# Optimization experiments

Measured on AMD Instinct MI355X. Metric: run time of the kernel, lower is better.

Reference implementation:

```python
import jax, jax.numpy as jnp
import numpy as np

B, T, H = 8, 4096, 512
K = 8192  # codebook size


def setup_inputs() -> dict:
    key = jax.random.key(0)
    kz, ke = jax.random.split(key)
    z = jax.random.normal(kz, (B, T, H), dtype=jnp.float32)
    emb = jax.random.normal(ke, (K, H), dtype=jnp.float32) * 0.02
    return {"z": z, "emb": emb}


def reference(z, emb):
    b, t, h = z.shape
    flat = z.reshape(b * t, h)
    dist = (jnp.sum(flat * flat, axis=1, keepdims=True)
            - 2.0 * (flat @ emb.T)
            + jnp.sum(emb * emb, axis=1)[None, :])
    idx = jnp.argmin(dist, axis=1)            # (b*t,)
    z_q = emb[idx].reshape(b, t, h)           # codebook lookup
    # straight-through estimator
    z_st = z + jax.lax.stop_gradient(z_q - z)
    codebook_loss = jnp.mean((z_q - jax.lax.stop_gradient(z)) ** 2)
    commit_loss = jnp.mean((z - jax.lax.stop_gradient(z_q)) ** 2)
    return z_st, idx.reshape(b, t), codebook_loss, commit_loss
```

## Files before the change

kernel.cpp:

```cpp
#include <hip/hip_runtime.h>
#include <cstdint>
#include <cstddef>

#define M_ROWS 32768
#define K_CODES 8192
#define H_DIM 512
#define TAU 2.5e-4f
#define MAXFLAG 32768

typedef float  f32x4 __attribute__((ext_vector_type(4)));
typedef short  s16x8 __attribute__((ext_vector_type(8)));

typedef __attribute__((address_space(3))) void as3_void;
typedef const __attribute__((address_space(1))) void as1_cvoid;
#define GLD16(gp, lp) __builtin_amdgcn_global_load_lds((as1_cvoid*)(gp), (as3_void*)(lp), 16, 0, 0)

__device__ __forceinline__ unsigned short f2bf(float f) {
    uint32_t u = __float_as_uint(f);
    u = u + 0x7fffu + ((u >> 16) & 1u);
    return (unsigned short)(u >> 16);
}
__device__ __forceinline__ float bf2f(unsigned short h) {
    return __uint_as_float(((uint32_t)h) << 16);
}

__device__ __forceinline__ float np_sumsq_row32(const float* row, int lane32) {
    const int c = lane32 >> 3, j = lane32 & 7;
    const float* p = row + c * 128 + j;
    float s = __fmul_rn(p[0], p[0]);
    #pragma unroll
    for (int t = 1; t < 16; ++t) {
        const float v = p[8 * t];
        s = __fadd_rn(s, __fmul_rn(v, v));
    }
    s = __fadd_rn(s, __shfl_xor(s, 1));
    s = __fadd_rn(s, __shfl_xor(s, 2));
    s = __fadd_rn(s, __shfl_xor(s, 4));
    s = __fadd_rn(s, __shfl_xor(s, 8));
    s = __fadd_rn(s, __shfl_xor(s, 16));
    return s;
}

__global__ __launch_bounds__(256) void prep_kernel(
    const float* __restrict__ z, const float* __restrict__ emb,
    unsigned short* __restrict__ zh, unsigned short* __restrict__ zl,
    unsigned short* __restrict__ eh, unsigned short* __restrict__ el,
    float* __restrict__ x2, float* __restrict__ e2,
    float* __restrict__ loss_slots, int* __restrict__ flag_count, int do_split)
{
    __shared__ float zr[8][512];
    const int row0 = blockIdx.x * 8;

    #pragma unroll
    for (int k = 0; k < 4; ++k) {
        const int f  = threadIdx.x + k * 256;
        const int r  = f >> 7;
        const int c4 = f & 127;
        const int grow = row0 + r;
        const float* src; unsigned short* hi; unsigned short* lo; size_t off;
        if (grow < M_ROWS) { src = z;   hi = zh; lo = zl; off = (size_t)grow * H_DIM; }
        else               { src = emb; hi = eh; lo = el; off = (size_t)(grow - M_ROWS) * H_DIM; }
        const float4 v = *reinterpret_cast<const float4*>(src + off + (size_t)c4 * 4);
        zr[r][c4 * 4 + 0] = v.x;
        zr[r][c4 * 4 + 1] = v.y;
        zr[r][c4 * 4 + 2] = v.z;
        zr[r][c4 * 4 + 3] = v.w;
        if (do_split) {
            ushort4 h, l;
            h.x = f2bf(v.x); l.x = f2bf(v.x - bf2f(h.x));
            h.y = f2bf(v.y); l.y = f2bf(v.y - bf2f(h.y));
            h.z = f2bf(v.z); l.z = f2bf(v.z - bf2f(h.z));
            h.w = f2bf(v.w); l.w = f2bf(v.w - bf2f(h.w));
            *reinterpret_cast<ushort4*>(hi + off + (size_t)c4 * 4) = h;
            *reinterpret_cast<ushort4*>(lo + off + (size_t)c4 * 4) = l;
        }
    }
    __syncthreads();

    const int r = threadIdx.x >> 5;
    const float s = np_sumsq_row32(&zr[r][0], threadIdx.x & 31);
    if ((threadIdx.x & 31) == 0) {
        const int grow = row0 + r;
        if (grow < M_ROWS) x2[grow] = s;
        else               e2[grow - M_ROWS] = s;
    }
    if (blockIdx.x == 0) {
        if (threadIdx.x < 2) loss_slots[threadIdx.x] = 0.f;
        if (threadIdx.x == 0) *flag_count = 0;
    }
}

__device__ __forceinline__ void top2_merge(float& b1, int& ix, float& b2,
                                           float ob1, int oix, float ob2) {
    if (ob1 < b1)      { b2 = fminf(b1, ob2); b1 = ob1; ix = oix; }
    else if (ob1 > b1) { b2 = fminf(b2, ob1); }
    else               { if (oix < ix) ix = oix; b2 = b1; }
}

__global__ __launch_bounds__(512, 1) void mfma_dist_kernel(
    const unsigned short* __restrict__ zh, const unsigned short* __restrict__ zl,
    const unsigned short* __restrict__ eh, const unsigned short* __restrict__ el,
    const float* __restrict__ x2, const float* __restrict__ e2,
    float* __restrict__ pb1, float* __restrict__ pb2, int* __restrict__ pidx)
{
    __shared__ __align__(16) unsigned short lb[2][4][8192];

    const int tid = threadIdx.x;
    const int l   = tid & 63;
    const int w   = tid >> 6;
    const int wm  = w >> 2;
    const int wn  = w & 3;

    const int bid  = blockIdx.x;
    const int xcd  = bid & 7;
    const int sq   = bid >> 3;
    const int band = sq >> 7;
    const int r128 = sq & 127;
    const int ct   = r128 >> 2;
    const int rt   = (band * 8 + xcd) * 4 + (r128 & 3);
    const int row0 = rt * 256;
    const int c0   = ct * 256;

    const int m    = w >> 1;
    const int half = w & 1;
    const unsigned short* sp = (m == 0) ? zh : (m == 1) ? zl : (m == 2) ? eh : el;
    const int rbase0 = (m < 2) ? row0 : c0;
    const unsigned short* sb = sp
        + (size_t)(rbase0 + half * 128 + (l >> 2)) * H_DIM
        + ((l & 3) ^ ((l >> 3) & 3)) * 8;

    const int aoff = (wm * 128 + (l & 15)) * 64 + (((l >> 4) ^ ((l >> 1) & 3)) * 16);
    const int boff = (wn * 64  + (l & 15)) * 64 + (((l >> 4) ^ ((l >> 1) & 3)) * 16);

    f32x4 acc[8][4];
    #pragma unroll
    for (int i = 0; i < 8; ++i)
        #pragma unroll
        for (int j = 0; j < 4; ++j)
            acc[i][j] = (f32x4){0.f, 0.f, 0.f, 0.f};

    {
        char* dst = (char*)&lb[0][m][0] + half * 8192;
        #pragma unroll
        for (int t = 0; t < 8; ++t)
            GLD16(sb + (size_t)t * 16 * H_DIM, dst + t * 1024);
    }
    asm volatile("s_waitcnt vmcnt(0)" ::: "memory");
    __builtin_amdgcn_s_barrier();

    for (int s = 0; s < 16; ++s) {
        const int par = s & 1;

        if (s < 15) {
            const unsigned short* src = sb + (s + 1) * 32;
            char* dst = (char*)&lb[par ^ 1][m][0] + half * 8192;
            #pragma unroll
            for (int t = 0; t < 8; ++t)
                GLD16(src + (size_t)t * 16 * H_DIM, dst + t * 1024);
            asm volatile("s_waitcnt vmcnt(8)" ::: "memory");
        } else {
            asm volatile("s_waitcnt vmcnt(0)" ::: "memory");
        }
        __builtin_amdgcn_s_barrier();

        const char* pAh = (const char*)&lb[par][0][0];
        const char* pAl = (const char*)&lb[par][1][0];
        const char* pBh = (const char*)&lb[par][2][0];
        const char* pBl = (const char*)&lb[par][3][0];

        s16x8 ah[8];
        #pragma unroll
        for (int i = 0; i < 8; ++i)
            ah[i] = *(const s16x8*)(pAh + aoff + i * 1024);
        s16x8 bh[4], bv[4];
        #pragma unroll
        for (int j = 0; j < 4; ++j) {
            bh[j] = *(const s16x8*)(pBh + boff + j * 1024);
            bv[j] = *(const s16x8*)(pBl + boff + j * 1024);
        }

        __builtin_amdgcn_s_setprio(1);
        #pragma unroll
        for (int j = 0; j < 4; ++j)
            #pragma unroll
            for (int i = 0; i < 8; ++i)
                acc[i][j] = __builtin_amdgcn_mfma_f32_16x16x32_bf16(ah[i], bv[j], acc[i][j], 0, 0, 0);
        s16x8 avA[4];
        #pragma unroll
        for (int i = 0; i < 4; ++i)
            avA[i] = *(const s16x8*)(pAl + aoff + i * 1024);
        #pragma unroll
        for (int j = 0; j < 4; ++j)
            #pragma unroll
            for (int i = 0; i < 8; ++i)
                acc[i][j] = __builtin_amdgcn_mfma_f32_16x16x32_bf16(ah[i], bh[j], acc[i][j], 0, 0, 0);
        s16x8 avB[4];
        #pragma unroll
        for (int i = 0; i < 4; ++i)
            avB[i] = *(const s16x8*)(pAl + aoff + (4 + i) * 1024);
        #pragma unroll
        for (int j = 0; j < 4; ++j)
            #pragma unroll
            for (int i = 0; i < 4; ++i)
                acc[i][j] = __builtin_amdgcn_mfma_f32_16x16x32_bf16(avA[i], bh[j], acc[i][j], 0, 0, 0);
        #pragma unroll
        for (int j = 0; j < 4; ++j)
            #pragma unroll
            for (int i = 0; i < 4; ++i)
                acc[4 + i][j] = __builtin_amdgcn_mfma_f32_16x16x32_bf16(avB[i], bh[j], acc[4 + i][j], 0, 0, 0);
        __builtin_amdgcn_s_setprio(0);

        __builtin_amdgcn_s_barrier();
    }

    float* mb1 = (float*)&lb[0][0][0];
    float* mb2 = mb1 + 1024;
    int*   mi  = (int*)(mb1 + 2048);

    float e2v[4];
    #pragma unroll
    for (int j = 0; j < 4; ++j)
        e2v[j] = e2[c0 + wn * 64 + j * 16 + (l & 15)];

    #pragma unroll
    for (int i = 0; i < 8; ++i) {
        const float4 x2v = *reinterpret_cast<const float4*>(
            x2 + row0 + wm * 128 + i * 16 + (l >> 4) * 4);
        const float x2a[4] = {x2v.x, x2v.y, x2v.z, x2v.w};
        #pragma unroll
        for (int r = 0; r < 4; ++r) {
            float b1 = 3.4e38f, b2 = 3.4e38f; int ix = 0;
            #pragma unroll
            for (int j = 0; j < 4; ++j) {
                const float d = __fadd_rn(__fmaf_rn(-2.f, acc[i][j][r], x2a[r]), e2v[j]);
                const int cj = c0 + wn * 64 + j * 16 + (l & 15);
                if (d < b1)      { b2 = b1; b1 = d; ix = cj; }
                else if (d < b2) { b2 = d; }
            }
            #pragma unroll
            for (int mm = 1; mm <= 8; mm <<= 1) {
                const float ob1 = __shfl_xor(b1, mm);
                const float ob2 = __shfl_xor(b2, mm);
                const int   oix = __shfl_xor(ix, mm);
                top2_merge(b1, ix, b2, ob1, oix, ob2);
            }
            if ((l & 15) == 0) {
                const int rl = wm * 128 + i * 16 + (l >> 4) * 4 + r;
                mb1[wn * 256 + rl] = b1;
                mb2[wn * 256 + rl] = b2;
                mi [wn * 256 + rl] = ix;
            }
        }
    }
    __syncthreads();
    if (tid < 256) {
        float b1 = mb1[tid], b2 = mb2[tid]; int ix = mi[tid];
        #pragma unroll
        for (int q = 1; q < 4; ++q)
            top2_merge(b1, ix, b2, mb1[q * 256 + tid], mi[q * 256 + tid], mb2[q * 256 + tid]);
        const size_t o = (size_t)ct * M_ROWS + row0 + tid;
        pb1[o] = b1; pb2[o] = b2; pidx[o] = ix;
    }
}

__global__ __launch_bounds__(256) void combine_kernel(
    const float* __restrict__ pb1, const float* __restrict__ pb2,
    const int* __restrict__ pidx,
    int* __restrict__ idx_i, float* __restrict__ idx_f,
    int* __restrict__ flag_count, int* __restrict__ flag_rows)
{
    const int r = blockIdx.x * 256 + threadIdx.x;
    if (r >= M_ROWS) return;
    float b1 = pb1[r], b2 = pb2[r]; int ix = pidx[r];
    #pragma unroll 4
    for (int ct = 1; ct < 32; ++ct)
        top2_merge(b1, ix, b2, pb1[(size_t)ct * M_ROWS + r],
                   pidx[(size_t)ct * M_ROWS + r], pb2[(size_t)ct * M_ROWS + r]);
    idx_i[r] = ix;
    idx_f[r] = (float)ix;
    if (b2 - b1 < TAU) {
        const int p = atomicAdd(flag_count, 1);
        if (p < MAXFLAG) flag_rows[p] = r;
    }
}

#define BM 64
#define BN 128
#define BH 32
#define PADZ 4
#define PADE 4

__device__ __forceinline__ void stage_transposed(const float* __restrict__ src,
                                                 int row0, int h0,
                                                 float* lds, int R, int ldp) {
    const int nf4 = R * (BH / 4);
    for (int f = threadIdx.x; f < nf4; f += 256) {
        const int r  = f / (BH / 4);
        const int c4 = (f % (BH / 4)) * 4;
        const float4 v = *reinterpret_cast<const float4*>(
            src + (size_t)(row0 + r) * H_DIM + h0 + c4);
        lds[(c4 + 0) * ldp + r] = v.x;
        lds[(c4 + 1) * ldp + r] = v.y;
        lds[(c4 + 2) * ldp + r] = v.z;
        lds[(c4 + 3) * ldp + r] = v.w;
    }
}

__global__ __launch_bounds__(256) void dist_argmin_kernel(
    const float* __restrict__ z, const float* __restrict__ emb,
    const float* __restrict__ x2, const float* __restrict__ e2,
    int* __restrict__ idx_i, float* __restrict__ idx_f,
    int* __restrict__ flag_count, int* __restrict__ flag_rows)
{
    __shared__ float zs[BH * (BM + PADZ)];
    __shared__ float es[BH * (BN + PADE)];
    __shared__ float bd[BM][17];
    __shared__ float bd2[BM][17];
    __shared__ int   bi[BM][17];

    const int row0 = blockIdx.x * BM;
    const int tx = threadIdx.x & 15;
    const int ty = threadIdx.x >> 4;

    float x2r[4];
    #pragma unroll
    for (int i = 0; i < 4; ++i) x2r[i] = x2[row0 + ty * 4 + i];

    float best[4], best2[4];
    int   bidx[4];
    #pragma unroll
    for (int i = 0; i < 4; ++i) { best[i] = 3.4e38f; best2[i] = 3.4e38f; bidx[i] = 0; }

    for (int nt = 0; nt < K_CODES / BN; ++nt) {
        float acc[4][8];
        #pragma unroll
        for (int i = 0; i < 4; ++i)
            #pragma unroll
            for (int j = 0; j < 8; ++j) acc[i][j] = 0.f;

        for (int hc = 0; hc < H_DIM / BH; ++hc) {
            __syncthreads();
            stage_transposed(z,   row0,    hc * BH, zs, BM, BM + PADZ);
            stage_transposed(emb, nt * BN, hc * BH, es, BN, BN + PADE);
            __syncthreads();
            #pragma unroll
            for (int h = 0; h < BH; ++h) {
                const float4 zr = *reinterpret_cast<const float4*>(&zs[h * (BM + PADZ) + ty * 4]);
                const float4 e0 = *reinterpret_cast<const float4*>(&es[h * (BN + PADE) + tx * 4]);
                const float4 e1 = *reinterpret_cast<const float4*>(&es[h * (BN + PADE) + 64 + tx * 4]);
                const float zrv[4] = {zr.x, zr.y, zr.z, zr.w};
                const float ev[8]  = {e0.x, e0.y, e0.z, e0.w, e1.x, e1.y, e1.z, e1.w};
                #pragma unroll
                for (int i = 0; i < 4; ++i)
                    #pragma unroll
                    for (int j = 0; j < 8; ++j)
                        acc[i][j] = fmaf(zrv[i], ev[j], acc[i][j]);
            }
        }
        #pragma unroll
        for (int j = 0; j < 8; ++j) {
            const int code = nt * BN + (j < 4 ? tx * 4 + j : 64 + tx * 4 + (j - 4));
            const float e2v = e2[code];
            #pragma unroll
            for (int i = 0; i < 4; ++i) {
                const float d = __fadd_rn(__fmaf_rn(-2.f, acc[i][j], x2r[i]), e2v);
                if (d < best[i])       { best2[i] = best[i]; best[i] = d; bidx[i] = code; }
                else if (d < best2[i]) { best2[i] = d; }
            }
        }
    }

    __syncthreads();
    #pragma unroll
    for (int i = 0; i < 4; ++i) {
        bd [ty * 4 + i][tx] = best[i];
        bd2[ty * 4 + i][tx] = best2[i];
        bi [ty * 4 + i][tx] = bidx[i];
    }
    __syncthreads();
    if (threadIdx.x < BM) {
        const int r = threadIdx.x;
        float g1 = bd[r][0]; int gi = bi[r][0]; float g2 = bd2[r][0];
        #pragma unroll
        for (int t = 1; t < 16; ++t) {
            const float v = bd[r][t]; const int x = bi[r][t];
            if (v < g1)       { g2 = g1; g1 = v; gi = x; }
            else if (v == g1) { g2 = g1; if (x < gi) gi = x; }
            else              { g2 = fminf(g2, v); }
            g2 = fminf(g2, bd2[r][t]);
        }
        idx_i[row0 + r] = gi;
        idx_f[row0 + r] = (float)gi;
        if (g2 - g1 < TAU) {
            const int p = atomicAdd(flag_count, 1);
            if (p < MAXFLAG) flag_rows[p] = row0 + r;
        }
    }
}

__global__ __launch_bounds__(256) void fixup_scan_kernel(
    const float* __restrict__ z, const float* __restrict__ emb,
    const float* __restrict__ x2, const float* __restrict__ e2,
    const int* __restrict__ flag_count, const int* __restrict__ flag_rows,
    float* __restrict__ qb1, int* __restrict__ qix)
{
    __shared__ float zrow[H_DIM];
    __shared__ float sd[256];
    __shared__ int   si[256];
    int n = *flag_count; if (n > MAXFLAG) n = MAXFLAG;
    const int q = blockIdx.x & 3;
    for (int j = blockIdx.x >> 2; j < n; j += (gridDim.x >> 2)) {
        const int row = flag_rows[j];
        __syncthreads();
        for (int h = threadIdx.x; h < H_DIM; h += 256)
            zrow[h] = z[(size_t)row * H_DIM + h];
        __syncthreads();
        const float x2r = x2[row];
        float bdv = 3.4e38f; int biv = 0x7fffffff;
        for (int k = q * 2048 + threadIdx.x; k < q * 2048 + 2048; k += 256) {
            const float* ek = emb + (size_t)k * H_DIM;
            double d0 = 0.0, d1 = 0.0, d2 = 0.0, d3 = 0.0;
            for (int h = 0; h < H_DIM; h += 4) {
                const float4 ev = *reinterpret_cast<const float4*>(ek + h);
                const float4 zv = *reinterpret_cast<const float4*>(&zrow[h]);
                d0 = fma((double)zv.x, (double)ev.x, d0);
                d1 = fma((double)zv.y, (double)ev.y, d1);
                d2 = fma((double)zv.z, (double)ev.z, d2);
                d3 = fma((double)zv.w, (double)ev.w, d3);
            }
            const float gf = (float)((d0 + d1) + (d2 + d3));
            const float d = __fadd_rn(__fmaf_rn(-2.f, gf, x2r), e2[k]);
            if (d < bdv) { bdv = d; biv = k; }
        }
        sd[threadIdx.x] = bdv; si[threadIdx.x] = biv;
        __syncthreads();
        for (int s = 128; s; s >>= 1) {
            if (threadIdx.x < s) {
                const float od = sd[threadIdx.x + s]; const int oi = si[threadIdx.x + s];
                if (od < sd[threadIdx.x] ||
                    (od == sd[threadIdx.x] && oi < si[threadIdx.x])) {
                    sd[threadIdx.x] = od; si[threadIdx.x] = oi;
                }
            }
            __syncthreads();
        }
        if (threadIdx.x == 0) { qb1[j * 4 + q] = sd[0]; qix[j * 4 + q] = si[0]; }
        __syncthreads();
    }
}

__global__ __launch_bounds__(256) void fixup_merge_kernel(
    const int* __restrict__ flag_count, const int* __restrict__ flag_rows,
    const float* __restrict__ qb1, const int* __restrict__ qix,
    int* __restrict__ idx_i, float* __restrict__ idx_f)
{
    int n = *flag_count; if (n > MAXFLAG) n = MAXFLAG;
    const int t = blockIdx.x * 256 + threadIdx.x;
    if (t >= n) return;
    float b = qb1[t * 4]; int ix = qix[t * 4];
    #pragma unroll
    for (int q = 1; q < 4; ++q) {
        const float ob = qb1[t * 4 + q];
        if (ob < b) { b = ob; ix = qix[t * 4 + q]; }
    }
    idx_i[flag_rows[t]] = ix;
    idx_f[flag_rows[t]] = (float)ix;
}

__global__ __launch_bounds__(256) void epilogue_kernel(
    const float* __restrict__ z, const float* __restrict__ emb,
    const int* __restrict__ idx_i,
    float* __restrict__ z_st, float* __restrict__ loss_slots)
{
    const int NQ = M_ROWS * (H_DIM / 4);
    const float4* z4 = reinterpret_cast<const float4*>(z);
    const float4* e4 = reinterpret_cast<const float4*>(emb);
    float4* o4 = reinterpret_cast<float4*>(z_st);
    float local = 0.f;
    for (int q = blockIdx.x * 256 + threadIdx.x; q < NQ; q += gridDim.x * 256) {
        const int r  = q >> 7;
        const int h4 = q & 127;
        const float4 zq = e4[(size_t)idx_i[r] * 128 + h4];
        const float4 zv = z4[q];
        float4 t, o;
        t.x = zq.x - zv.x; o.x = zv.x + t.x;
        t.y = zq.y - zv.y; o.y = zv.y + t.y;
        t.z = zq.z - zv.z; o.z = zv.z + t.z;
        t.w = zq.w - zv.w; o.w = zv.w + t.w;
        o4[q] = o;
        local = fmaf(t.x, t.x, local);
        local = fmaf(t.y, t.y, local);
        local = fmaf(t.z, t.z, local);
        local = fmaf(t.w, t.w, local);
    }
    #pragma unroll
    for (int off = 32; off; off >>= 1) local += __shfl_down(local, off);
    __shared__ float part[4];
    const int lane = threadIdx.x & 63, wid = threadIdx.x >> 6;
    if (lane == 0) part[wid] = local;
    __syncthreads();
    if (threadIdx.x == 0) {
        const float s = (part[0] + part[1] + part[2] + part[3])
                        * (1.f / (float)((size_t)M_ROWS * H_DIM));
        atomicAdd(&loss_slots[0], s);
        atomicAdd(&loss_slots[1], s);
    }
}

extern "C" void kernel_launch(void* const* d_in, const int* in_sizes, int n_in,
                              void* d_out, int out_size, void* d_ws, size_t ws_size,
                              hipStream_t stream) {
    const float* z   = (const float*)d_in[0];
    const float* emb = (const float*)d_in[1];

    float* out   = (float*)d_out;
    float* z_st  = out;
    float* idx_f = out + (size_t)M_ROWS * H_DIM;
    float* loss  = out + (size_t)M_ROWS * H_DIM + M_ROWS;

    float* pb1  = z_st;
    float* pb2  = z_st + (size_t)32 * M_ROWS;
    int*   pidx = (int*)(z_st + (size_t)64 * M_ROWS);
    float* qb1  = z_st + (size_t)96 * M_ROWS;
    int*   qix  = (int*)(z_st + (size_t)96 * M_ROWS + 4 * MAXFLAG);

    char* ws = (char*)d_ws;
    float* e2     = (float*)(ws + 0);
    float* x2     = (float*)(ws + 32768);
    int*   idx_i  = (int*)  (ws + 163840);
    int*   fcount = (int*)  (ws + 294912);
    int*   frows  = (int*)  (ws + 294976);
    unsigned short* zh = (unsigned short*)(ws + 426048);
    unsigned short* zl = (unsigned short*)(ws + 426048 + 33554432ull);
    unsigned short* eh = (unsigned short*)(ws + 426048 + 67108864ull);
    unsigned short* el = (unsigned short*)(ws + 426048 + 75497472ull);
    const size_t REQ = 426048ull + 83886080ull;

    const int use_mfma = (ws_size >= REQ) ? 1 : 0;

    hipLaunchKernelGGL(prep_kernel, dim3((M_ROWS + K_CODES) / 8), dim3(256), 0, stream,
                       z, emb, zh, zl, eh, el, x2, e2, loss, fcount, use_mfma);

    if (use_mfma) {
        hipLaunchKernelGGL(mfma_dist_kernel, dim3(4096), dim3(512), 0, stream,
                           zh, zl, eh, el, x2, e2, pb1, pb2, pidx);
        hipLaunchKernelGGL(combine_kernel, dim3(M_ROWS / 256), dim3(256), 0, stream,
                           pb1, pb2, pidx, idx_i, idx_f, fcount, frows);
    } else {
        hipLaunchKernelGGL(dist_argmin_kernel, dim3(M_ROWS / BM), dim3(256), 0, stream,
                           z, emb, x2, e2, idx_i, idx_f, fcount, frows);
    }

    hipLaunchKernelGGL(fixup_scan_kernel, dim3(8192), dim3(256), 0, stream,
                       z, emb, x2, e2, fcount, frows, qb1, qix);
    hipLaunchKernelGGL(fixup_merge_kernel, dim3(MAXFLAG / 256), dim3(256), 0, stream,
                       fcount, frows, qb1, qix, idx_i, idx_f);
    hipLaunchKernelGGL(epilogue_kernel, dim3(2048), dim3(256), 0, stream,
                       z, emb, idx_i, z_st, loss);
}
```

Baseline: 1.170 ms.

## Split GEMM k-step into four phases interleaving LDS reads, prefetch and MFMA

Restructures the main distance-GEMM loop into four sub-phases. Each phase loads two A fragments (high and low bf16 parts), issues part of the next-stage global-to-LDS prefetch, and then runs the MFMAs for those rows, fencing with barriers and sched_barrier. The aim is to overlap LDS reads and global prefetch with MFMA work and to lower register pressure by holding fewer A fragments at once. The cost is more barriers per iteration. The prefetch now waits with vmcnt(0) at the end of each iteration instead of partway through. It also drops the lo-by-lo-free term ordering for rows 4-7 and computes all three split-bf16 products per row.

```diff
diff --git a/kernel.cpp b/kernel.cpp
--- a/kernel.cpp
+++ b/kernel.cpp
@@ -148,70 +148,105 @@
     asm volatile("s_waitcnt vmcnt(0)" ::: "memory");
     __builtin_amdgcn_s_barrier();
 
+#define MFMA_PAIR(I0, AH0, AV0, AH1, AV1)                                                        \
+    _Pragma("unroll")                                                                            \
+    for (int j = 0; j < 4; ++j) {                                                                \
+        acc[I0][j]     = __builtin_amdgcn_mfma_f32_16x16x32_bf16(AV0, bh[j], acc[I0][j], 0,0,0); \
+        acc[I0][j]     = __builtin_amdgcn_mfma_f32_16x16x32_bf16(AH0, bv[j], acc[I0][j], 0,0,0); \
+        acc[I0][j]     = __builtin_amdgcn_mfma_f32_16x16x32_bf16(AH0, bh[j], acc[I0][j], 0,0,0); \
+        acc[I0+1][j]   = __builtin_amdgcn_mfma_f32_16x16x32_bf16(AV1, bh[j], acc[I0+1][j], 0,0,0); \
+        acc[I0+1][j]   = __builtin_amdgcn_mfma_f32_16x16x32_bf16(AH1, bv[j], acc[I0+1][j], 0,0,0); \
+        acc[I0+1][j]   = __builtin_amdgcn_mfma_f32_16x16x32_bf16(AH1, bh[j], acc[I0+1][j], 0,0,0); \
+    }
+
     for (int s = 0; s < 16; ++s) {
         const int par = s & 1;
-
-        if (s < 15) {
-            const unsigned short* src = sb + (s + 1) * 32;
-            char* dst = (char*)&lb[par ^ 1][m][0] + half * 8192;
-            #pragma unroll
-            for (int t = 0; t < 8; ++t)
-                GLD16(src + (size_t)t * 16 * H_DIM, dst + t * 1024);
-            asm volatile("s_waitcnt vmcnt(8)" ::: "memory");
-        } else {
-            asm volatile("s_waitcnt vmcnt(0)" ::: "memory");
-        }
-        __builtin_amdgcn_s_barrier();
-
         const char* pAh = (const char*)&lb[par][0][0];
         const char* pAl = (const char*)&lb[par][1][0];
         const char* pBh = (const char*)&lb[par][2][0];
         const char* pBl = (const char*)&lb[par][3][0];
-
-        s16x8 ah[8];
-        #pragma unroll
-        for (int i = 0; i < 8; ++i)
-            ah[i] = *(const s16x8*)(pAh + aoff + i * 1024);
+        char* dst = (char*)&lb[par ^ 1][m][0] + half * 8192;
+        const unsigned short* src = sb + (s + 1) * 32;
+        const bool pf = (s < 15);
+
         s16x8 bh[4], bv[4];
-        #pragma unroll
-        for (int j = 0; j < 4; ++j) {
-            bh[j] = *(const s16x8*)(pBh + boff + j * 1024);
-            bv[j] = *(const s16x8*)(pBl + boff + j * 1024);
-        }
-
-        __builtin_amdgcn_s_setprio(1);
-        #pragma unroll
-        for (int j = 0; j < 4; ++j)
+
+        {
             #pragma unroll
-            for (int i = 0; i < 8; ++i)
-                acc[i][j] = __builtin_amdgcn_mfma_f32_16x16x32_bf16(ah[i], bv[j], acc[i][j], 0, 0, 0);
-        s16x8 avA[4];
-        #pragma unroll
-        for (int i = 0; i < 4; ++i)
-            avA[i] = *(const s16x8*)(pAl + aoff + i * 1024);
-        #pragma unroll
-        for (int j = 0; j < 4; ++j)
-            #pragma unroll
-            for (int i = 0; i < 8; ++i)
-                acc[i][j] = __builtin_amdgcn_mfma_f32_16x16x32_bf16(ah[i], bh[j], acc[i][j], 0, 0, 0);
-        s16x8 avB[4];
-        #pragma unroll
-        for (int i = 0; i < 4; ++i)
-            avB[i] = *(const s16x8*)(pAl + aoff + (4 + i) * 1024);
-        #pragma unroll
-        for (int j = 0; j < 4; ++j)
-            #pragma unroll
-            for (int i = 0; i < 4; ++i)
-                acc[i][j] = __builtin_amdgcn_mfma_f32_16x16x32_bf16(avA[i], bh[j], acc[i][j], 0, 0, 0);
-        #pragma unroll
-        for (int j = 0; j < 4; ++j)
-            #pragma unroll
-            for (int i = 0; i < 4; ++i)
-                acc[4 + i][j] = __builtin_amdgcn_mfma_f32_16x16x32_bf16(avB[i], bh[j], acc[4 + i][j], 0, 0, 0);
-        __builtin_amdgcn_s_setprio(0);
-
-        __builtin_amdgcn_s_barrier();
-    }
+            for (int j = 0; j < 4; ++j) {
+                bh[j] = *(const s16x8*)(pBh + boff + j * 1024);
+                bv[j] = *(const s16x8*)(pBl + boff + j * 1024);
+            }
+            const s16x8 a0h = *(const s16x8*)(pAh + aoff + 0 * 1024);
+            const s16x8 a0v = *(const s16x8*)(pAl + aoff + 0 * 1024);
+            const s16x8 a1h = *(const s16x8*)(pAh + aoff + 1 * 1024);
+            const s16x8 a1v = *(const s16x8*)(pAl + aoff + 1 * 1024);
+            if (pf) {
+                GLD16(src + (size_t)0 * 16 * H_DIM, dst + 0 * 1024);
+                GLD16(src + (size_t)1 * 16 * H_DIM, dst + 1 * 1024);
+                GLD16(src + (size_t)2 * 16 * H_DIM, dst + 2 * 1024);
+                GLD16(src + (size_t)3 * 16 * H_DIM, dst + 3 * 1024);
+            }
+            __builtin_amdgcn_sched_barrier(0);
+            __builtin_amdgcn_s_barrier();
+            asm volatile("s_waitcnt lgkmcnt(0)" ::: "memory");
+            __builtin_amdgcn_sched_barrier(0);
+            __builtin_amdgcn_s_setprio(1);
+            MFMA_PAIR(0, a0h, a0v, a1h, a1v)
+            __builtin_amdgcn_s_setprio(0);
+            __builtin_amdgcn_s_barrier();
+        }
+        {
+            const s16x8 a0h = *(const s16x8*)(pAh + aoff + 2 * 1024);
+            const s16x8 a0v = *(const s16x8*)(pAl + aoff + 2 * 1024);
+            const s16x8 a1h = *(const s16x8*)(pAh + aoff + 3 * 1024);
+            const s16x8 a1v = *(const s16x8*)(pAl + aoff + 3 * 1024);
+            if (pf) {
+                GLD16(src + (size_t)4 * 16 * H_DIM, dst + 4 * 1024);
+                GLD16(src + (size_t)5 * 16 * H_DIM, dst + 5 * 1024);
+                GLD16(src + (size_t)6 * 16 * H_DIM, dst + 6 * 1024);
+                GLD16(src + (size_t)7 * 16 * H_DIM, dst + 7 * 1024);
+            }
+            __builtin_amdgcn_sched_barrier(0);
+            __builtin_amdgcn_s_barrier();
+            asm volatile("s_waitcnt lgkmcnt(0)" ::: "memory");
+            __builtin_amdgcn_sched_barrier(0);
+            __builtin_amdgcn_s_setprio(1);
+            MFMA_PAIR(2, a0h, a0v, a1h, a1v)
+            __builtin_amdgcn_s_setprio(0);
+            __builtin_amdgcn_s_barrier();
+        }
+        {
+            const s16x8 a0h = *(const s16x8*)(pAh + aoff + 4 * 1024);
+            const s16x8 a0v = *(const s16x8*)(pAl + aoff + 4 * 1024);
+            const s16x8 a1h = *(const s16x8*)(pAh + aoff + 5 * 1024);
+            const s16x8 a1v = *(const s16x8*)(pAl + aoff + 5 * 1024);
+            __builtin_amdgcn_sched_barrier(0);
+            __builtin_amdgcn_s_barrier();
+            asm volatile("s_waitcnt lgkmcnt(0)" ::: "memory");
+            __builtin_amdgcn_sched_barrier(0);
+            __builtin_amdgcn_s_setprio(1);
+            MFMA_PAIR(4, a0h, a0v, a1h, a1v)
+            __builtin_amdgcn_s_setprio(0);
+            __builtin_amdgcn_s_barrier();
+        }
+        {
+            const s16x8 a0h = *(const s16x8*)(pAh + aoff + 6 * 1024);
+            const s16x8 a0v = *(const s16x8*)(pAl + aoff + 6 * 1024);
+            const s16x8 a1h = *(const s16x8*)(pAh + aoff + 7 * 1024);
+            const s16x8 a1v = *(const s16x8*)(pAl + aoff + 7 * 1024);
+            __builtin_amdgcn_sched_barrier(0);
+            __builtin_amdgcn_s_barrier();
+            asm volatile("s_waitcnt lgkmcnt(0)" ::: "memory");
+            __builtin_amdgcn_sched_barrier(0);
+            __builtin_amdgcn_s_setprio(1);
+            MFMA_PAIR(6, a0h, a0v, a1h, a1v)
+            __builtin_amdgcn_s_setprio(0);
+            asm volatile("s_waitcnt vmcnt(0)" ::: "memory");
+            __builtin_amdgcn_s_barrier();
+        }
+    }
+#undef MFMA_PAIR
 
     float* mb1 = (float*)&lb[0][0][0];
     float* mb2 = mb1 + 1024;
```

Result: faster. 1.142 ms (-2.3%).
